# Performance work log

Hardware: AMD Instinct MI355X
Metric: run time of the kernel (lower is better)

The kernel has to match this reference:

```python
import jax, jax.numpy as jnp
import numpy as np

B, C, H, W = 4, 64, 128, 128
G, K, PAD, DIL = 4, 3, 2, 2  # deformable conv config
OFF_CH = 2 * K * K * G  # 72


def conv2d(x, w, b, pad):
    out = jax.lax.conv_general_dilated(
        x, w, window_strides=(1, 1), padding=[(pad, pad), (pad, pad)],
        dimension_numbers=('NCHW', 'OIHW', 'NCHW'))
    return out + b[None, :, None, None]


def deform_conv(x, offset, w, b):
    # DCNv1 (no modulation mask), groups=G, offset_groups=G, torchvision semantics.
    Bn, Cn, Hn, Wn = x.shape
    Cg = Cn // G
    Cout = w.shape[0]
    Coutg = Cout // G
    # offset channels laid out as [G, K*K, (dy,dx)]
    off = offset.reshape(Bn, G, K * K, 2, Hn, Wn)
    dy, dx = off[:, :, :, 0], off[:, :, :, 1]  # [B,G,9,H,W]
    kk = jnp.arange(K * K)
    gy = (jnp.arange(Hn)[None, :] - PAD + DIL * (kk // K)[:, None]).astype(x.dtype)[:, :, None]  # [9,H,1]
    gx = (jnp.arange(Wn)[None, :] - PAD + DIL * (kk % K)[:, None]).astype(x.dtype)[:, None, :]   # [9,1,W]
    py = dy + gy[None, None]  # [B,G,9,H,W]
    px = dx + gx[None, None]
    xg = x.reshape(Bn, G, Cg, Hn, Wn)

    def gather(img, py_, px_):  # img [Cg,H,W]; py_,px_ [9,H,W]
        y0 = jnp.floor(py_)
        x0 = jnp.floor(px_)
        ly = py_ - y0
        lx = px_ - x0

        def corner(iy, ix, wgt):
            valid = (iy >= 0) & (iy <= Hn - 1) & (ix >= 0) & (ix <= Wn - 1)
            iyc = jnp.clip(iy, 0, Hn - 1).astype(jnp.int32)
            ixc = jnp.clip(ix, 0, Wn - 1).astype(jnp.int32)
            return img[:, iyc, ixc] * (wgt * valid)[None]

        return (corner(y0, x0, (1 - ly) * (1 - lx))
                + corner(y0, x0 + 1, (1 - ly) * lx)
                + corner(y0 + 1, x0, ly * (1 - lx))
                + corner(y0 + 1, x0 + 1, ly * lx))

    sampled = jax.vmap(jax.vmap(gather))(xg, py, px)  # [B,G,Cg,9,H,W]
    wr = w.reshape(G, Coutg, Cg, K * K)
    out = jnp.einsum('bgckhw,gock->bgohw', sampled, wr).reshape(Bn, Cout, Hn, Wn)
    return out + b[None, :, None, None]


def setup_inputs() -> dict:
    key = jax.random.key(0)
    ks = jax.random.split(key, 32)
    f32 = jnp.float32
    d = {
        'Fref': jax.random.normal(ks[0], (B, C, H, W), f32),
        'Fmov1': jax.random.normal(ks[1], (B, C, H, W), f32),
        'Fmov2': jax.random.normal(ks[2], (B, C, H, W), f32),
        'cr_w': jax.random.normal(ks[3], (64, 128, 3, 3), f32) * 0.05,
        'cr_b': jax.random.normal(ks[4], (64,), f32) * 0.05,
    }
    i = 5
    for name in ('off1', 'off2', 'off3', 'off4'):
        d[name + '_w'] = jax.random.normal(ks[i], (OFF_CH, 64, 3, 3), f32) * 0.01
        d[name + '_b'] = jax.random.normal(ks[i + 1], (OFF_CH,), f32) * 0.01
        i += 2
    for name in ('d1', 'd2', 'd3', 'd4'):
        d[name + '_w'] = jax.random.normal(ks[i], (64, 64 // G, 3, 3), f32) * 0.05
        d[name + '_b'] = jax.random.normal(ks[i + 1], (64,), f32) * 0.05
        i += 2
    return d


def reference(Fref, Fmov1, Fmov2, cr_w, cr_b,
              off1_w, off1_b, off2_w, off2_b, off3_w, off3_b, off4_w, off4_b,
              d1_w, d1_b, d2_w, d2_b, d3_w, d3_b, d4_w, d4_b):
    def align(fr, fm):
        fea = conv2d(jnp.concatenate([fr, fm], axis=1), cr_w, cr_b, 1)
        fea = deform_conv(fea, conv2d(fea, off1_w, off1_b, 1), d1_w, d1_b)
        fea = deform_conv(fea, conv2d(fea, off2_w, off2_b, 1), d2_w, d2_b)
        off3 = conv2d(fea, off3_w, off3_b, 1)
        fea = deform_conv(fm, off3, d3_w, d3_b)  # note: deform3 applied to Fmov, per source
        out = deform_conv(fea, conv2d(fea, off4_w, off4_b, 1), d4_w, d4_b)
        return out

    return (align(Fref, Fmov1), align(Fref, Fmov2))
```

## Files before the change

### kernel.cpp

```cpp
#include <hip/hip_runtime.h>


using f16   = _Float16;
using f16x8 = __attribute__((ext_vector_type(8))) f16;
using h2    = __attribute__((ext_vector_type(2))) f16;
using u16x8 = __attribute__((ext_vector_type(8))) unsigned short;
using f32x4 = __attribute__((ext_vector_type(4))) float;

static constexpr int Hh = 128, Ww = 128, NB = 4, NPIX = Hh * Ww;
static constexpr int BB = 8;

__device__ __forceinline__ unsigned short f2h(float f) {
  f16 h = (f16)f;
  return *(unsigned short*)&h;
}

struct PrepPtrs {
  const float* cw[5];
  unsigned short* cd[5];
  const float* dw[4];
  unsigned short* dd[4];
  const float* ob[4];
  float* obd[4];
};

__global__ __launch_bounds__(256) void prep_all_kernel(PrepPtrs pp) {
  const int which = blockIdx.y;
  const int i = blockIdx.x * 256 + threadIdx.x;
  if (which == 0) {
    if (i >= 9 * 64 * 128) return;
    const int cin = 128, cop = 64;
    const int ci = i % cin, co = (i / cin) % cop, t = i / (cin * cop);
    pp.cd[0][i] = f2h(pp.cw[0][((size_t)co * cin + ci) * 9 + t]);
  } else if (which <= 4) {
    if (i >= 9 * 80 * 64) return;
    const int cin = 64, cop = 80;
    const int ci = i % cin, co = (i / cin) % cop, t = i / (cin * cop);
    const int g = co / 20, c = co % 20;
    float v = (c < 18) ? pp.cw[which][((size_t)(g * 18 + c) * cin + ci) * 9 + t]
                       : 0.f;
    pp.cd[which][i] = f2h(v);
  } else if (which <= 8) {
    if (i >= 4 * 5 * 16 * 32) return;
    const int kk = i & 31, o = (i >> 5) & 15, pair = (i >> 9) % 5;
    const int g = i / 2560;
    const int t = pair * 2 + (kk >> 4), c = kk & 15;
    float v = (t < 9) ? pp.dw[which - 5][(size_t)((g * 16 + o) * 16 + c) * 9 + t]
                      : 0.f;
    pp.dd[which - 5][i] = f2h(v);
  } else {
    if (i >= 4 * 80) return;
    const int ten = i / 80, co = i % 80;
    const int g = co / 20, c = co % 20;
    pp.obd[ten][co] = (c < 18) ? pp.ob[ten][g * 18 + c] : 0.f;
  }
}

__global__ __launch_bounds__(256) void to_gs_kernel(
    const float* __restrict__ Fref, const float* __restrict__ Fm1,
    const float* __restrict__ Fm2, unsigned short* __restrict__ frefG,
    unsigned short* __restrict__ fmovG) {
  const int t = blockIdx.x * 256 + threadIdx.x;
  const int b2 = t >> 14, pix = t & (NPIX - 1);
  const float* fm = (b2 < 4 ? Fm1 : Fm2) + (size_t)(b2 & 3) * 64 * NPIX + pix;
  for (int c8 = 0; c8 < 8; ++c8) {
    u16x8 v;
#pragma unroll
    for (int j = 0; j < 8; ++j) v[j] = f2h(fm[(size_t)(c8 * 8 + j) * NPIX]);
    *(u16x8*)(fmovG + ((size_t)(b2 * 4 + (c8 >> 1)) * NPIX + pix) * 16 +
              (c8 & 1) * 8) = v;
  }
  if (b2 < 4) {
    const float* fr = Fref + (size_t)b2 * 64 * NPIX + pix;
    for (int c8 = 0; c8 < 8; ++c8) {
      u16x8 v;
#pragma unroll
      for (int j = 0; j < 8; ++j) v[j] = f2h(fr[(size_t)(c8 * 8 + j) * NPIX]);
      *(u16x8*)(frefG + ((size_t)(b2 * 4 + (c8 >> 1)) * NPIX + pix) * 16 +
                (c8 & 1) * 8) = v;
    }
  }
}

template <int CIN, int COP, int CO_REAL>
__global__ __launch_bounds__(512, 2) void convmfma_kernel(
    const unsigned short* __restrict__ in0, int bmask0,
    const unsigned short* __restrict__ in1, int bmask1,
    const unsigned short* __restrict__ wT,
    const float* __restrict__ biasP,
    unsigned short* __restrict__ out) {
  constexpr int COF = COP / 16;
  constexpr int NCH = CIN / 64;
  constexpr int NT = NCH * 9;
  __shared__ unsigned short sW[2][COP * 64];
  __shared__ unsigned short sB[324 * 64];

  const int tile = blockIdx.x, b = blockIdx.y;
  const int ty0 = (tile >> 3) << 4, tx0 = (tile & 7) << 4;
  const int tid = threadIdx.x;
  const int wv = tid >> 6, l = tid & 63;
  const int lm = l & 15, lq = l >> 4;

  f32x4 acc[COF][2];
#pragma unroll
  for (int cf = 0; cf < COF; ++cf)
#pragma unroll
    for (int pf = 0; pf < 2; ++pf) acc[cf][pf] = (f32x4){0.f, 0.f, 0.f, 0.f};

  const unsigned short* base0 = in0 + (size_t)(b & bmask0) * 4 * NPIX * 16;
  const unsigned short* base1 =
      (NCH > 1) ? in1 + (size_t)(b & bmask1) * 4 * NPIX * 16 : nullptr;

  auto stage_input = [&](int ch) {
    const unsigned short* inB = (ch == 0) ? base0 : base1;
    for (int q = tid; q < 324 * 8; q += 512) {
      const int pix = q >> 3, ci8 = q & 7;
      const int r = pix / 18, c = pix - r * 18;
      const int gy = ty0 - 1 + r, gx = tx0 - 1 + c;
      u16x8 v;
      if (gy >= 0 && gy < Hh && gx >= 0 && gx < Ww) {
        v = *(const u16x8*)(inB + ((size_t)(ci8 >> 1) * NPIX + gy * Ww + gx) *
                                      16 + (ci8 & 1) * 8);
      } else {
#pragma unroll
        for (int j = 0; j < 8; ++j) v[j] = 0;
      }
      const int boff = pix * 128 + ((ci8 * 16) ^ ((pix & 7) << 4));
      *(u16x8*)((char*)sB + boff) = v;
    }
  };
  auto stage_w = [&](int tt, int buf) {
    const int ch = tt / 9, t = tt - ch * 9;
    for (int q = tid; q < COP * 8; q += 512) {
      const int ci8 = q & 7;
      const int co = q >> 3;
      u16x8 v = *(const u16x8*)(wT + (size_t)(t * COP + co) * CIN + ch * 64 +
                                ci8 * 8);
      const int aoff = co * 128 + ((ci8 * 16) ^ ((co & 7) << 4));
      *(u16x8*)((char*)sW[buf] + aoff) = v;
    }
  };

  stage_input(0);
  stage_w(0, 0);
  __syncthreads();

  for (int tt = 0; tt < NT; ++tt) {
    const int t = tt % 9;
    const bool nextNewCh = ((tt + 1) % 9 == 0);
    if (tt + 1 < NT && !nextNewCh) stage_w(tt + 1, (tt + 1) & 1);

    const int dy = t / 3, dx = t - dy * 3;
    const char* sWc = (const char*)sW[tt & 1];
#pragma unroll
    for (int kc = 0; kc < 2; ++kc) {
      f16x8 afr[COF];
#pragma unroll
      for (int cf = 0; cf < COF; ++cf) {
        const int co = cf * 16 + lm;
        const int aoff = co * 128 + ((kc * 64 + lq * 16) ^ ((co & 7) << 4));
        afr[cf] = *(const f16x8*)(sWc + aoff);
      }
#pragma unroll
      for (int pf = 0; pf < 2; ++pf) {
        const int pix = wv * 32 + pf * 16 + lm;
        const int spix = ((pix >> 4) + dy) * 18 + (pix & 15) + dx;
        const int boff = spix * 128 + ((kc * 64 + lq * 16) ^ ((spix & 7) << 4));
        const f16x8 bfr = *(const f16x8*)((const char*)sB + boff);
#pragma unroll
        for (int cf = 0; cf < COF; ++cf)
          acc[cf][pf] = __builtin_amdgcn_mfma_f32_16x16x32_f16(
              afr[cf], bfr, acc[cf][pf], 0, 0, 0);
      }
    }
    __syncthreads();
    if (tt + 1 < NT && nextNewCh) {
      stage_input((tt + 1) / 9);
      stage_w(tt + 1, (tt + 1) & 1);
      __syncthreads();
    }
  }

#pragma unroll
  for (int cf = 0; cf < COF; ++cf) {
    const int co0 = cf * 16 + lq * 4;
    if (co0 >= CO_REAL) continue;
    const float4 bv = *(const float4*)(biasP + co0);
#pragma unroll
    for (int pf = 0; pf < 2; ++pf) {
      const int pix = wv * 32 + pf * 16 + lm;
      const int gpix = (ty0 + (pix >> 4)) * Ww + tx0 + (pix & 15);
      const f32x4 v = acc[cf][pf];
      ushort4 pk;
      pk.x = f2h(v[0] + bv.x);
      pk.y = f2h(v[1] + bv.y);
      pk.z = f2h(v[2] + bv.z);
      pk.w = f2h(v[3] + bv.w);
      const int gg = co0 >> 4, cc = co0 & 15;
      *(ushort4*)(out + ((size_t)(b * 4 + gg) * NPIX + gpix) * 16 + cc) = pk;
    }
  }
}

template <bool NCHW_OUT>
__global__ __launch_bounds__(256, 4) void fused_od_kernel(
    const unsigned short* __restrict__ convIn,
    const unsigned short* __restrict__ sampX,
    const unsigned short* __restrict__ wT,
    const float* __restrict__ obias,
    const unsigned short* __restrict__ dwP,
    const float* __restrict__ dbias,
    float* __restrict__ outF, unsigned short* __restrict__ outH) {
  __shared__ __attribute__((aligned(16))) char lds[36352];
  char* sB = lds;
  char* sW = lds + 26112;
  char* sOffB = lds;
  char* bounce = lds + 26112;

  const int tile = blockIdx.x, b = blockIdx.y;
  const int ty0 = (tile >> 2) << 2;
  const int tx0 = (tile & 3) << 5;
  const int tid = threadIdx.x;
  const int wv = tid >> 6, l = tid & 63;
  const int lm = l & 15, lq = l >> 4;

  f32x4 acc[5][2];
#pragma unroll
  for (int cf = 0; cf < 5; ++cf)
#pragma unroll
    for (int pf = 0; pf < 2; ++pf) acc[cf][pf] = (f32x4){0.f, 0.f, 0.f, 0.f};

  const unsigned short* inB = convIn + (size_t)b * 4 * NPIX * 16;

  u16x8 wr0, wr1, wr2;
  auto wload = [&](int t) {
    const unsigned short* wt = wT + (size_t)t * 5120;
    wr0 = *(const u16x8*)(wt + (size_t)(tid >> 3) * 64 + (tid & 7) * 8);
    const int q1 = tid + 256;
    wr1 = *(const u16x8*)(wt + (size_t)(q1 >> 3) * 64 + (q1 & 7) * 8);
    if (tid < 128) {
      const int q2 = tid + 512;
      wr2 = *(const u16x8*)(wt + (size_t)(q2 >> 3) * 64 + (q2 & 7) * 8);
    }
  };
  auto wstore = [&]() {
    auto put = [&](int q, u16x8 v) {
      const int co = q >> 3, ci8 = q & 7;
      *(u16x8*)(sW + co * 128 + ((ci8 * 16) ^ ((co & 7) << 4))) = v;
    };
    put(tid, wr0);
    put(tid + 256, wr1);
    if (tid < 128) put(tid + 512, wr2);
  };

  wload(0);
  for (int q = tid; q < 204 * 8; q += 256) {
    const int pix = q >> 3, ci8 = q & 7;
    const int r = pix / 34, c = pix - r * 34;
    const int gy = ty0 - 1 + r, gx = tx0 - 1 + c;
    u16x8 v;
    if (gy >= 0 && gy < Hh && gx >= 0 && gx < Ww) {
      v = *(const u16x8*)(inB + ((size_t)(ci8 >> 1) * NPIX + gy * Ww + gx) *
                                    16 + (ci8 & 1) * 8);
    } else {
#pragma unroll
      for (int j = 0; j < 8; ++j) v[j] = 0;
    }
    const int boff = pix * 128 + ((ci8 * 16) ^ ((pix & 7) << 4));
    *(u16x8*)(sB + boff) = v;
  }
  wstore();
  __syncthreads();

  for (int t = 0; t < 9; ++t) {
    if (t + 1 < 9) wload(t + 1);
    const int dy = t / 3, dx = t - dy * 3;
#pragma unroll
    for (int kc = 0; kc < 2; ++kc) {
      f16x8 afr[5];
#pragma unroll
      for (int cf = 0; cf < 5; ++cf) {
        const int co = cf * 16 + lm;
        const int aoff = co * 128 + ((kc * 64 + lq * 16) ^ ((co & 7) << 4));
        afr[cf] = *(const f16x8*)(sW + aoff);
      }
#pragma unroll
      for (int pf = 0; pf < 2; ++pf) {
        const int pix = wv * 32 + pf * 16 + lm;
        const int spix = ((pix >> 5) + dy) * 34 + (pix & 31) + dx;
        const int boff = spix * 128 + ((kc * 64 + lq * 16) ^ ((spix & 7) << 4));
        const f16x8 bfr = *(const f16x8*)(sB + boff);
#pragma unroll
        for (int cf = 0; cf < 5; ++cf)
          acc[cf][pf] = __builtin_amdgcn_mfma_f32_16x16x32_f16(
              afr[cf], bfr, acc[cf][pf], 0, 0, 0);
      }
    }
    __syncthreads();
    if (t + 1 < 9) {
      wstore();
      __syncthreads();
    }
  }

#pragma unroll
  for (int cf = 0; cf < 5; ++cf) {
    const int co0 = cf * 16 + lq * 4;
    const float4 bv = *(const float4*)(obias + co0);
#pragma unroll
    for (int pf = 0; pf < 2; ++pf) {
      const int pix = wv * 32 + pf * 16 + lm;
      const f32x4 v = acc[cf][pf];
      ushort4 pk;
      pk.x = f2h(v[0] + bv.x);
      pk.y = f2h(v[1] + bv.y);
      pk.z = f2h(v[2] + bv.z);
      pk.w = f2h(v[3] + bv.w);
      *(ushort4*)(sOffB + pix * 168 + co0 * 2) = pk;
    }
  }
  __syncthreads();

  const int p = tid >> 1, h = tid & 1;
  const int y = ty0 + (p >> 5), xx = tx0 + (p & 31);
  char* myB = bounce + p * 80 + h * 16;

  for (int g = 0; g < 4; ++g) {
    const unsigned short* xP =
        sampX + (size_t)(b * 4 + g) * NPIX * 16 + h * 8;
    unsigned od[9];
#pragma unroll
    for (int t = 0; t < 9; ++t)
      od[t] = *(const unsigned*)(sOffB + p * 168 + (g * 20 + 2 * t) * 2);

    f16x8 afr[5];
#pragma unroll
    for (int pr = 0; pr < 5; ++pr)
      afr[pr] = *(const f16x8*)(dwP + ((size_t)(g * 5 + pr) * 16 + lm) * 32 +
                                lq * 8);

    f32x4 dacc[2];
    dacc[0] = (f32x4){0.f, 0.f, 0.f, 0.f};
    dacc[1] = (f32x4){0.f, 0.f, 0.f, 0.f};

#pragma unroll
    for (int pair = 0; pair < 5; ++pair) {
#pragma unroll
      for (int ti = 0; ti < 2; ++ti) {
        const int t = pair * 2 + ti;
        uint4 sv = (uint4){0u, 0u, 0u, 0u};
        if (t < 9) {
          const unsigned odw = od[t];
          const f16* op = (const f16*)&odw;
          const float dy = (float)op[0];
          const float dx = (float)op[1];
          const float py = dy + (float)(y - 2 + 2 * (t / 3));
          const float px = dx + (float)(xx - 2 + 2 * (t % 3));
          const float fy = floorf(py), fx = floorf(px);
          const int y0 = (int)fy, x0 = (int)fx;
          const int y1 = y0 + 1, x1 = x0 + 1;
          const float ly = py - fy, lx = px - fx;
          float w00 = (1.f - ly) * (1.f - lx), w01 = (1.f - ly) * lx;
          float w10 = ly * (1.f - lx), w11 = ly * lx;
          const bool vy0 = (y0 >= 0) && (y0 < Hh), vy1 = (y1 >= 0) && (y1 < Hh);
          const bool vx0 = (x0 >= 0) && (x0 < Ww), vx1 = (x1 >= 0) && (x1 < Ww);
          w00 = (vy0 && vx0) ? w00 : 0.f;
          w01 = (vy0 && vx1) ? w01 : 0.f;
          w10 = (vy1 && vx0) ? w10 : 0.f;
          w11 = (vy1 && vx1) ? w11 : 0.f;
          const int y0c = min(max(y0, 0), Hh - 1), y1c = min(max(y1, 0), Hh - 1);
          const int x0c = min(max(x0, 0), Ww - 1), x1c = min(max(x1, 0), Ww - 1);
          const u16x8 a00 = *(const u16x8*)(xP + (size_t)(y0c * Ww + x0c) * 16);
          const u16x8 a01 = *(const u16x8*)(xP + (size_t)(y0c * Ww + x1c) * 16);
          const u16x8 a10 = *(const u16x8*)(xP + (size_t)(y1c * Ww + x0c) * 16);
          const u16x8 a11 = *(const u16x8*)(xP + (size_t)(y1c * Ww + x1c) * 16);
          const h2* c00 = (const h2*)&a00;
          const h2* c01 = (const h2*)&a01;
          const h2* c10 = (const h2*)&a10;
          const h2* c11 = (const h2*)&a11;
          const f16 h00 = (f16)w00, h01 = (f16)w01;
          const f16 h10 = (f16)w10, h11 = (f16)w11;
          const h2 p00 = (h2){h00, h00}, p01 = (h2){h01, h01};
          const h2 p10 = (h2){h10, h10}, p11 = (h2){h11, h11};
          unsigned fw[4];
#pragma unroll
          for (int j = 0; j < 4; ++j) {
            h2 r = c00[j] * p00;
            r += c01[j] * p01;
            r += c10[j] * p10;
            r += c11[j] * p11;
            fw[j] = *(const unsigned*)&r;
          }
          sv = (uint4){fw[0], fw[1], fw[2], fw[3]};
        }
        *(uint4*)(myB + ti * 32) = sv;
      }
#pragma unroll
      for (int n = 0; n < 2; ++n) {
        const f16x8 bfr =
            *(const f16x8*)(bounce + (wv * 32 + n * 16 + lm) * 80 + lq * 16);
        dacc[n] = __builtin_amdgcn_mfma_f32_16x16x32_f16(afr[pair], bfr,
                                                         dacc[n], 0, 0, 0);
      }
    }

    const float4 bv = *(const float4*)(dbias + g * 16 + lq * 4);
#pragma unroll
    for (int n = 0; n < 2; ++n) {
      const int pixl = wv * 32 + n * 16 + lm;
      const int gpix = (ty0 + (pixl >> 5)) * Ww + tx0 + (pixl & 31);
      const f32x4 v = dacc[n];
      if (NCHW_OUT) {
        float* oB = outF + (size_t)(b * 64 + g * 16 + lq * 4) * NPIX + gpix;
        oB[0] = v[0] + bv.x;
        oB[NPIX] = v[1] + bv.y;
        oB[2 * NPIX] = v[2] + bv.z;
        oB[3 * NPIX] = v[3] + bv.w;
      } else {
        ushort4 pk;
        pk.x = f2h(v[0] + bv.x);
        pk.y = f2h(v[1] + bv.y);
        pk.z = f2h(v[2] + bv.z);
        pk.w = f2h(v[3] + bv.w);
        *(ushort4*)(outH + ((size_t)(b * 4 + g) * NPIX + gpix) * 16 + lq * 4) =
            pk;
      }
    }
  }
}


extern "C" void kernel_launch(void* const* d_in, const int* in_sizes, int n_in,
                              void* d_out, int out_size, void* d_ws,
                              size_t ws_size, hipStream_t stream) {
  const float* Fref = (const float*)d_in[0];
  const float* Fmov1 = (const float*)d_in[1];
  const float* Fmov2 = (const float*)d_in[2];
  const float* cr_w = (const float*)d_in[3];
  const float* cr_b = (const float*)d_in[4];
  const float* offw[4] = {(const float*)d_in[5], (const float*)d_in[7],
                          (const float*)d_in[9], (const float*)d_in[11]};
  const float* offb[4] = {(const float*)d_in[6], (const float*)d_in[8],
                          (const float*)d_in[10], (const float*)d_in[12]};
  const float* dw[4] = {(const float*)d_in[13], (const float*)d_in[15],
                        (const float*)d_in[17], (const float*)d_in[19]};
  const float* db[4] = {(const float*)d_in[14], (const float*)d_in[16],
                        (const float*)d_in[18], (const float*)d_in[20]};

  char* p = (char*)d_ws;
  auto carve = [&](size_t bytes) {
    void* r = p;
    p += (bytes + 255) & ~(size_t)255;
    return r;
  };
  unsigned short* frefG = (unsigned short*)carve((size_t)4 * 4 * NPIX * 16 * 2);
  unsigned short* fmovG = (unsigned short*)carve((size_t)BB * 4 * NPIX * 16 * 2);
  unsigned short* feaA = (unsigned short*)carve((size_t)BB * 4 * NPIX * 16 * 2);
  unsigned short* feaB = (unsigned short*)carve((size_t)BB * 4 * NPIX * 16 * 2);
  unsigned short* wcrT = (unsigned short*)carve((size_t)9 * 64 * 128 * 2);
  unsigned short* woffT[4];
  for (int i = 0; i < 4; ++i)
    woffT[i] = (unsigned short*)carve((size_t)9 * 80 * 64 * 2);
  unsigned short* dwP[4];
  for (int i = 0; i < 4; ++i)
    dwP[i] = (unsigned short*)carve((size_t)4 * 5 * 16 * 32 * 2);
  float* obP[4];
  for (int i = 0; i < 4; ++i) obP[i] = (float*)carve((size_t)80 * 4);

  PrepPtrs pp;
  pp.cw[0] = cr_w;
  pp.cd[0] = wcrT;
  for (int i = 0; i < 4; ++i) {
    pp.cw[i + 1] = offw[i];
    pp.cd[i + 1] = woffT[i];
    pp.dw[i] = dw[i];
    pp.dd[i] = dwP[i];
    pp.ob[i] = offb[i];
    pp.obd[i] = obP[i];
  }
  prep_all_kernel<<<dim3(288, 10), 256, 0, stream>>>(pp);

  to_gs_kernel<<<BB * NPIX / 256, 256, 0, stream>>>(Fref, Fmov1, Fmov2, frefG,
                                                    fmovG);

  const dim3 cgrid(64, BB), cblk(512);
  const dim3 fgrid(128, BB), fblk(256);
  float* outF = (float*)d_out;

  convmfma_kernel<128, 64, 64><<<cgrid, cblk, 0, stream>>>(
      frefG, 3, fmovG, 7, wcrT, cr_b, feaA);
  fused_od_kernel<false><<<fgrid, fblk, 0, stream>>>(
      feaA, feaA, woffT[0], obP[0], dwP[0], db[0], nullptr, feaB);
  fused_od_kernel<false><<<fgrid, fblk, 0, stream>>>(
      feaB, feaB, woffT[1], obP[1], dwP[1], db[1], nullptr, feaA);
  fused_od_kernel<false><<<fgrid, fblk, 0, stream>>>(
      feaA, fmovG, woffT[2], obP[2], dwP[2], db[2], nullptr, feaB);
  fused_od_kernel<true><<<fgrid, fblk, 0, stream>>>(
      feaB, feaB, woffT[3], obP[3], dwP[3], db[3], outF, nullptr);
}
```

Measured before the change: 235.7 us.

## Load conv weight fragments directly from global memory instead of staging through LDS

Both the plain conv kernel and the fused offset/deform kernel now read MFMA weight fragments straight from global memory (through L1/L2) instead of double-buffering weights in shared memory. This removes the weight LDS buffers and the per-tap __syncthreads barriers. The freed shared memory is used to raise the launch-bound occupancy hints (2 to 6 blocks and 4 to 5 blocks). The cost is that every wave issues its own global loads for weights, so MFMA issue can stall on cache latency, and the tighter register budget from the higher occupancy targets may cause spills.

```diff
diff --git a/kernel.cpp b/kernel.cpp
--- a/kernel.cpp
+++ b/kernel.cpp
@@ -83,7 +83,7 @@
 }
 
 template <int CIN, int COP, int CO_REAL>
-__global__ __launch_bounds__(512, 2) void convmfma_kernel(
+__global__ __launch_bounds__(512, 6) void convmfma_kernel(
     const unsigned short* __restrict__ in0, int bmask0,
     const unsigned short* __restrict__ in1, int bmask1,
     const unsigned short* __restrict__ wT,
@@ -91,8 +91,6 @@
     unsigned short* __restrict__ out) {
   constexpr int COF = COP / 16;
   constexpr int NCH = CIN / 64;
-  constexpr int NT = NCH * 9;
-  __shared__ unsigned short sW[2][COP * 64];
   __shared__ unsigned short sB[324 * 64];
 
   const int tile = blockIdx.x, b = blockIdx.y;
@@ -111,8 +109,9 @@
   const unsigned short* base1 =
       (NCH > 1) ? in1 + (size_t)(b & bmask1) * 4 * NPIX * 16 : nullptr;
 
-  auto stage_input = [&](int ch) {
+  for (int ch = 0; ch < NCH; ++ch) {
     const unsigned short* inB = (ch == 0) ? base0 : base1;
+    if (ch) __syncthreads();
     for (int q = tid; q < 324 * 8; q += 512) {
       const int pix = q >> 3, ci8 = q & 7;
       const int r = pix / 18, c = pix - r * 18;
@@ -128,56 +127,32 @@
       const int boff = pix * 128 + ((ci8 * 16) ^ ((pix & 7) << 4));
       *(u16x8*)((char*)sB + boff) = v;
     }
-  };
-  auto stage_w = [&](int tt, int buf) {
-    const int ch = tt / 9, t = tt - ch * 9;
-    for (int q = tid; q < COP * 8; q += 512) {
-      const int ci8 = q & 7;
-      const int co = q >> 3;
-      u16x8 v = *(const u16x8*)(wT + (size_t)(t * COP + co) * CIN + ch * 64 +
-                                ci8 * 8);
-      const int aoff = co * 128 + ((ci8 * 16) ^ ((co & 7) << 4));
-      *(u16x8*)((char*)sW[buf] + aoff) = v;
-    }
-  };
-
-  stage_input(0);
-  stage_w(0, 0);
-  __syncthreads();
-
-  for (int tt = 0; tt < NT; ++tt) {
-    const int t = tt % 9;
-    const bool nextNewCh = ((tt + 1) % 9 == 0);
-    if (tt + 1 < NT && !nextNewCh) stage_w(tt + 1, (tt + 1) & 1);
-
-    const int dy = t / 3, dx = t - dy * 3;
-    const char* sWc = (const char*)sW[tt & 1];
-#pragma unroll
-    for (int kc = 0; kc < 2; ++kc) {
-      f16x8 afr[COF];
-#pragma unroll
-      for (int cf = 0; cf < COF; ++cf) {
-        const int co = cf * 16 + lm;
-        const int aoff = co * 128 + ((kc * 64 + lq * 16) ^ ((co & 7) << 4));
-        afr[cf] = *(const f16x8*)(sWc + aoff);
-      }
-#pragma unroll
-      for (int pf = 0; pf < 2; ++pf) {
-        const int pix = wv * 32 + pf * 16 + lm;
-        const int spix = ((pix >> 4) + dy) * 18 + (pix & 15) + dx;
-        const int boff = spix * 128 + ((kc * 64 + lq * 16) ^ ((spix & 7) << 4));
-        const f16x8 bfr = *(const f16x8*)((const char*)sB + boff);
-#pragma unroll
-        for (int cf = 0; cf < COF; ++cf)
-          acc[cf][pf] = __builtin_amdgcn_mfma_f32_16x16x32_f16(
-              afr[cf], bfr, acc[cf][pf], 0, 0, 0);
-      }
-    }
     __syncthreads();
-    if (tt + 1 < NT && nextNewCh) {
-      stage_input((tt + 1) / 9);
-      stage_w(tt + 1, (tt + 1) & 1);
-      __syncthreads();
+
+    for (int t = 0; t < 9; ++t) {
+      const int dy = t / 3, dx = t - dy * 3;
+      const unsigned short* wt = wT + (size_t)t * COP * CIN + ch * 64 + lq * 8;
+#pragma unroll
+      for (int kc = 0; kc < 2; ++kc) {
+        f16x8 afr[COF];
+#pragma unroll
+        for (int cf = 0; cf < COF; ++cf) {
+          const int co = cf * 16 + lm;
+          afr[cf] = *(const f16x8*)(wt + (size_t)co * CIN + kc * 32);
+        }
+#pragma unroll
+        for (int pf = 0; pf < 2; ++pf) {
+          const int pix = wv * 32 + pf * 16 + lm;
+          const int spix = ((pix >> 4) + dy) * 18 + (pix & 15) + dx;
+          const int boff =
+              spix * 128 + ((kc * 64 + lq * 16) ^ ((spix & 7) << 4));
+          const f16x8 bfr = *(const f16x8*)((const char*)sB + boff);
+#pragma unroll
+          for (int cf = 0; cf < COF; ++cf)
+            acc[cf][pf] = __builtin_amdgcn_mfma_f32_16x16x32_f16(
+                afr[cf], bfr, acc[cf][pf], 0, 0, 0);
+        }
+      }
     }
   }
 
@@ -203,7 +178,7 @@
 }
 
 template <bool NCHW_OUT>
-__global__ __launch_bounds__(256, 4) void fused_od_kernel(
+__global__ __launch_bounds__(256, 5) void fused_od_kernel(
     const unsigned short* __restrict__ convIn,
     const unsigned short* __restrict__ sampX,
     const unsigned short* __restrict__ wT,
@@ -211,11 +186,10 @@
     const unsigned short* __restrict__ dwP,
     const float* __restrict__ dbias,
     float* __restrict__ outF, unsigned short* __restrict__ outH) {
-  __shared__ __attribute__((aligned(16))) char lds[36352];
+  __shared__ __attribute__((aligned(16))) char lds[31744];
   char* sB = lds;
-  char* sW = lds + 26112;
   char* sOffB = lds;
-  char* bounce = lds + 26112;
+  char* bounce = lds + 21504;
 
   const int tile = blockIdx.x, b = blockIdx.y;
   const int ty0 = (tile >> 2) << 2;
@@ -232,28 +206,6 @@
 
   const unsigned short* inB = convIn + (size_t)b * 4 * NPIX * 16;
 
-  u16x8 wr0, wr1, wr2;
-  auto wload = [&](int t) {
-    const unsigned short* wt = wT + (size_t)t * 5120;
-    wr0 = *(const u16x8*)(wt + (size_t)(tid >> 3) * 64 + (tid & 7) * 8);
-    const int q1 = tid + 256;
-    wr1 = *(const u16x8*)(wt + (size_t)(q1 >> 3) * 64 + (q1 & 7) * 8);
-    if (tid < 128) {
-      const int q2 = tid + 512;
-      wr2 = *(const u16x8*)(wt + (size_t)(q2 >> 3) * 64 + (q2 & 7) * 8);
-    }
-  };
-  auto wstore = [&]() {
-    auto put = [&](int q, u16x8 v) {
-      const int co = q >> 3, ci8 = q & 7;
-      *(u16x8*)(sW + co * 128 + ((ci8 * 16) ^ ((co & 7) << 4))) = v;
-    };
-    put(tid, wr0);
-    put(tid + 256, wr1);
-    if (tid < 128) put(tid + 512, wr2);
-  };
-
-  wload(0);
   for (int q = tid; q < 204 * 8; q += 256) {
     const int pix = q >> 3, ci8 = q & 7;
     const int r = pix / 34, c = pix - r * 34;
@@ -269,20 +221,18 @@
     const int boff = pix * 128 + ((ci8 * 16) ^ ((pix & 7) << 4));
     *(u16x8*)(sB + boff) = v;
   }
-  wstore();
   __syncthreads();
 
   for (int t = 0; t < 9; ++t) {
-    if (t + 1 < 9) wload(t + 1);
     const int dy = t / 3, dx = t - dy * 3;
+    const unsigned short* wt = wT + (size_t)t * 5120 + lq * 8;
 #pragma unroll
     for (int kc = 0; kc < 2; ++kc) {
       f16x8 afr[5];
 #pragma unroll
       for (int cf = 0; cf < 5; ++cf) {
         const int co = cf * 16 + lm;
-        const int aoff = co * 128 + ((kc * 64 + lq * 16) ^ ((co & 7) << 4));
-        afr[cf] = *(const f16x8*)(sW + aoff);
+        afr[cf] = *(const f16x8*)(wt + (size_t)co * 64 + kc * 32);
       }
 #pragma unroll
       for (int pf = 0; pf < 2; ++pf) {
@@ -296,12 +246,8 @@
               afr[cf], bfr, acc[cf][pf], 0, 0, 0);
       }
     }
-    __syncthreads();
-    if (t + 1 < 9) {
-      wstore();
-      __syncthreads();
-    }
-  }
+  }
+  __syncthreads();
 
 #pragma unroll
   for (int cf = 0; cf < 5; ++cf) {
```

New measurement: 439.7 us. 86.6% more time.
